# Optimization experiments

Hardware: AMD Instinct MI355X
Metric: run time of the kernel (lower is better)

Reference implementation:

```python
import jax, jax.numpy as jnp
import numpy as np

COST_CLASS = 1.0


def _lsa(cost):
    """linear_sum_assignment clone (Jonker-Volgenant shortest augmenting path),
    matching scipy.optimize.linear_sum_assignment semantics for rectangular inputs."""
    cost = np.asarray(cost, dtype=np.float64)
    transposed = cost.shape[0] > cost.shape[1]
    if transposed:
        cost = cost.T
    nr, nc = cost.shape
    u = np.zeros(nr)
    v = np.zeros(nc)
    path = np.full(nc, -1, dtype=np.int64)
    col4row = np.full(nr, -1, dtype=np.int64)
    row4col = np.full(nc, -1, dtype=np.int64)
    for cur in range(nr):
        i = cur
        SR = np.zeros(nr, dtype=bool)
        SC = np.zeros(nc, dtype=bool)
        d = np.full(nc, np.inf)
        minVal = 0.0
        sink = -1
        while sink == -1:
            SR[i] = True
            rem = ~SC
            r = minVal + cost[i, rem] - u[i] - v[rem]
            dr = d[rem]
            pr = path[rem]
            better = r < dr
            dr[better] = r[better]
            pr[better] = i
            d[rem] = dr
            path[rem] = pr
            remIdx = np.flatnonzero(rem)
            j = remIdx[np.argmin(d[remIdx])]
            minVal = d[j]
            SC[j] = True
            if row4col[j] == -1:
                sink = j
            else:
                i = row4col[j]
        # dual updates (scipy _lsap_body)
        u[cur] += minVal
        mask = SR.copy()
        mask[cur] = False
        u[mask] += minVal - d[col4row[mask]]
        v[SC] -= minVal - d[SC]
        # augment along shortest path
        j = sink
        while True:
            i = path[j]
            row4col[j] = i
            col4row[i], j = j, col4row[i]
            if i == cur:
                break
    if transposed:
        order = np.argsort(col4row)
        return col4row[order], order
    return np.arange(nr), col4row


def setup_inputs() -> dict:
    key = jax.random.key(0)
    k1, k2, k3 = jax.random.split(key, 3)
    bs, Q, T, NC = 32, 256, 128, 2048
    pred_logits = jax.random.normal(k1, (bs, Q, NC), dtype=jnp.float32)
    tgt_labels = jax.random.randint(k2, (bs, T), 0, NC)
    agent_mask = jax.random.randint(k3, (bs, Q), 0, 2).astype(bool)
    return {"pred_logits": pred_logits, "tgt_labels": tgt_labels,
            "agent_mask": agent_mask, "use_background": 0}


def reference(pred_logits, tgt_labels, agent_mask, use_background):
    bs, Q, _ = pred_logits.shape
    T = tgt_labels.shape[1]
    probs = jax.nn.softmax(pred_logits, axis=-1)  # [bs, Q, NC]
    if not use_background:
        probs = jnp.where(agent_mask[:, :, None], probs, 0.0)
    out_prob = probs.reshape(bs * Q, -1)
    tgt_ids = tgt_labels.reshape(-1)                  # concat of all batch labels
    C = COST_CLASS * (-out_prob[:, tgt_ids])          # [bs*Q, bs*T]
    C = C.reshape(bs, Q, bs * T)
    # per-batch Hungarian (same as scipy loop in the original; inherently serial per instance)
    Cn = np.asarray(C)
    rows = np.empty((bs, T), dtype=np.int64)
    cols = np.empty((bs, T), dtype=np.int64)
    for i in range(bs):
        r, c = _lsa(Cn[i, :, i * T:(i + 1) * T])      # [Q, T] block for batch i
        rows[i] = r
        cols[i] = c
    return C, jnp.asarray(rows), jnp.asarray(cols)
```

## Files before the change

kernel.cpp:

```cpp
#include <hip/hip_runtime.h>
#include <hip/hip_bf16.h>
#include <math.h>

#define BS 32
#define QN 256
#define TN 128
#define NCLS 2048
#define NTGT (BS * TN)

__global__ void detect_mask_layout(const unsigned char* __restrict__ m, int* flag) {
    __shared__ int found;
    if (threadIdx.x == 0) found = 0;
    __syncthreads();
    int local = 0;
    for (int i = threadIdx.x; i < BS * QN; i += blockDim.x) {
        if ((i & 3) != 0 && m[i] != 0) local = 1;
    }
    if (local) atomicOr(&found, 1);
    __syncthreads();
    if (threadIdx.x == 0) *flag = found;
}

__global__ __launch_bounds__(256) void ct_kernel(
    const float* __restrict__ logits, const int* __restrict__ labels,
    const unsigned char* __restrict__ mask_b, const int* __restrict__ use_bg,
    const int* __restrict__ layout_flag, float* __restrict__ CT) {
    __shared__ float prob_sh[NCLS];
    __shared__ float red[4];

    const int tid = threadIdx.x;
    const int bq = blockIdx.x;
    const float* row = logits + (size_t)bq * NCLS;

    const float4 xa = ((const float4*)row)[tid];
    const float4 xb = ((const float4*)row)[tid + 256];

    float m = fmaxf(fmaxf(fmaxf(xa.x, xa.y), fmaxf(xa.z, xa.w)),
                    fmaxf(fmaxf(xb.x, xb.y), fmaxf(xb.z, xb.w)));
#pragma unroll
    for (int off = 32; off >= 1; off >>= 1) m = fmaxf(m, __shfl_xor(m, off));
    if ((tid & 63) == 0) red[tid >> 6] = m;
    __syncthreads();
    m = fmaxf(fmaxf(red[0], red[1]), fmaxf(red[2], red[3]));
    __syncthreads();

    float4 ea, eb;
    ea.x = expf(xa.x - m);
    ea.y = expf(xa.y - m);
    ea.z = expf(xa.z - m);
    ea.w = expf(xa.w - m);
    eb.x = expf(xb.x - m);
    eb.y = expf(xb.y - m);
    eb.z = expf(xb.z - m);
    eb.w = expf(xb.w - m);
    float s = ((ea.x + ea.y) + (ea.z + ea.w)) + ((eb.x + eb.y) + (eb.z + eb.w));
#pragma unroll
    for (int off = 32; off >= 1; off >>= 1) s += __shfl_xor(s, off);
    if ((tid & 63) == 0) red[tid >> 6] = s;
    __syncthreads();
    s = ((red[0] + red[1]) + red[2]) + red[3];

    ((float4*)prob_sh)[tid] = make_float4(ea.x / s, ea.y / s, ea.z / s, ea.w / s);
    ((float4*)prob_sh)[tid + 256] = make_float4(eb.x / s, eb.y / s, eb.z / s, eb.w / s);

    const int ub = *use_bg;
    int am;
    if (*layout_flag)
        am = mask_b[bq];
    else
        am = ((const int*)mask_b)[bq];
    const bool zero_row = (ub == 0) && (am == 0);
    __syncthreads();

    if (tid < TN) {
        const int bb = bq >> 8;
        const int q = bq & 255;
        const int lab = labels[bb * TN + tid];
        CT[(size_t)bb * TN * QN + (size_t)tid * QN + q] =
            zero_row ? 0.0f : -prob_sh[lab];
    }
}

__global__ __launch_bounds__(256) void compute_C_kernel(
    const float* __restrict__ logits, const int* __restrict__ labels,
    const unsigned char* __restrict__ mask_b, const int* __restrict__ use_bg,
    const int* __restrict__ layout_flag, float* __restrict__ C) {
    __shared__ float prob_sh[NCLS];
    __shared__ float red[4];

    const int tid = threadIdx.x;
    const int bq = blockIdx.x;
    const float* row = logits + (size_t)bq * NCLS;

    const float4 xa = ((const float4*)row)[tid];
    const float4 xb = ((const float4*)row)[tid + 256];

    float m = fmaxf(fmaxf(fmaxf(xa.x, xa.y), fmaxf(xa.z, xa.w)),
                    fmaxf(fmaxf(xb.x, xb.y), fmaxf(xb.z, xb.w)));
#pragma unroll
    for (int off = 32; off >= 1; off >>= 1) m = fmaxf(m, __shfl_xor(m, off));
    if ((tid & 63) == 0) red[tid >> 6] = m;
    __syncthreads();
    m = fmaxf(fmaxf(red[0], red[1]), fmaxf(red[2], red[3]));
    __syncthreads();

    float4 ea, eb;
    ea.x = expf(xa.x - m);
    ea.y = expf(xa.y - m);
    ea.z = expf(xa.z - m);
    ea.w = expf(xa.w - m);
    eb.x = expf(xb.x - m);
    eb.y = expf(xb.y - m);
    eb.z = expf(xb.z - m);
    eb.w = expf(xb.w - m);
    float s = ((ea.x + ea.y) + (ea.z + ea.w)) + ((eb.x + eb.y) + (eb.z + eb.w));
#pragma unroll
    for (int off = 32; off >= 1; off >>= 1) s += __shfl_xor(s, off);
    if ((tid & 63) == 0) red[tid >> 6] = s;
    __syncthreads();
    s = ((red[0] + red[1]) + red[2]) + red[3];

    ((float4*)prob_sh)[tid] = make_float4(ea.x / s, ea.y / s, ea.z / s, ea.w / s);
    ((float4*)prob_sh)[tid + 256] = make_float4(eb.x / s, eb.y / s, eb.z / s, eb.w / s);

    const int ub = *use_bg;
    int am;
    if (*layout_flag)
        am = mask_b[bq];
    else
        am = ((const int*)mask_b)[bq];
    const bool zero_row = (ub == 0) && (am == 0);
    __syncthreads();

    float* Crow = C + (size_t)bq * NTGT;
    const int4* lab4 = (const int4*)labels;
    if (zero_row) {
        const float4 z = make_float4(0.f, 0.f, 0.f, 0.f);
#pragma unroll
        for (int k = 0; k < 4; k++) ((float4*)Crow)[tid + k * 256] = z;
    } else {
#pragma unroll
        for (int k = 0; k < 4; k++) {
            const int4 l = lab4[tid + k * 256];
            float4 o;
            o.x = -prob_sh[l.x];
            o.y = -prob_sh[l.y];
            o.z = -prob_sh[l.z];
            o.w = -prob_sh[l.w];
            ((float4*)Crow)[tid + k * 256] = o;
        }
    }
}

template <int CTRL>
__device__ __forceinline__ double dpp_mov_f64(double x) {
    union { double d; int i[2]; } a, r;
    a.d = x;
    r.i[0] = __builtin_amdgcn_update_dpp(0, a.i[0], CTRL, 0xF, 0xF, true);
    r.i[1] = __builtin_amdgcn_update_dpp(0, a.i[1], CTRL, 0xF, 0xF, true);
    return r.d;
}
__device__ __forceinline__ double read_lane_f64(double x, int srclane) {
    union { double d; int i[2]; } a, r;
    a.d = x;
    r.i[0] = __builtin_amdgcn_readlane(a.i[0], srclane);
    r.i[1] = __builtin_amdgcn_readlane(a.i[1], srclane);
    return r.d;
}

#define QUAD_XOR1 0xB1
#define QUAD_XOR2 0x4E
#define ROW_ROR4  0x124
#define ROW_ROR8  0x128

__device__ __forceinline__ void lsa_solve(
    const float* __restrict__ C, const float* __restrict__ CT,
    float* __restrict__ rows_out, float* __restrict__ cols_out,
    int b, int lane,
    float* cost_sh, double* u_sh, int* path_sh, int* row4col_sh, int* col4row_sh) {
    const int j0 = lane * 4;

    u_sh[lane] = 0.0;
    u_sh[lane + 64] = 0.0;
    col4row_sh[lane] = -1;
    col4row_sh[lane + 64] = -1;
#pragma unroll
    for (int t = 0; t < 4; t++) row4col_sh[lane + 64 * t] = -1;

    double v0 = 0.0, v1 = 0.0, v2 = 0.0, v3 = 0.0;
    double u0 = 0.0, u1 = 0.0;

    if (CT) {
        const float4* src = (const float4*)(CT + (size_t)b * TN * QN);
        float4* dst = (float4*)cost_sh;
#pragma unroll 8
        for (int it = 0; it < TN * QN / 4 / 64; it++) {
            const int idx = it * 64 + lane;
            dst[idx] = src[idx];
        }
    } else {
        const float* cbsrc = C + (size_t)b * QN * NTGT + b * TN;
        for (int it = 0; it < 512; it++) {
            const int j = it >> 1;
            const int i = lane + 64 * (it & 1);
            cost_sh[i * QN + j] = cbsrc[(size_t)j * NTGT + i];
        }
    }
    __syncthreads();

    for (int cur = 0; cur < TN; cur++) {
        double dv0 = INFINITY, dv1 = INFINITY, dv2 = INFINITY, dv3 = INFINITY;
        double dm0 = INFINITY, dm1 = INFINITY, dm2 = INFINITY, dm3 = INFINITY;
        double du0 = 0.0, du1 = 0.0;
        int sc = 0, sr = 0;
        int p0 = 0, p1 = 0, p2 = 0, p3 = 0;
        const int4 rcv = *(const int4*)&row4col_sh[j0];
        if (lane == (cur >> 1)) sr = 1 << (cur & 1);

        int i = cur;
        double m_d = 0.0;
        bool need_reduce = true;
        unsigned long long B0 = 0, B1 = 0, B2 = 0, B3 = 0;
        int sink;

        while (true) {
            const float4 cc = *(const float4*)(cost_sh + i * QN + j0);
            const double ui = u_sh[i];

            const double ca0 = ((m_d + (double)cc.x) - ui) - v0;
            const double ca1 = ((m_d + (double)cc.y) - ui) - v1;
            const double ca2 = ((m_d + (double)cc.z) - ui) - v2;
            const double ca3 = ((m_d + (double)cc.w) - ui) - v3;
            const bool i0 = !(sc & 1) && (ca0 < dv0);
            const bool i1 = !(sc & 2) && (ca1 < dv1);
            const bool i2 = !(sc & 4) && (ca2 < dv2);
            const bool i3 = !(sc & 8) && (ca3 < dv3);
            const unsigned long long anyI =
                __ballot(i0) | __ballot(i1) | __ballot(i2) | __ballot(i3);
            if (i0) { dv0 = ca0; dm0 = ca0; p0 = i; }
            if (i1) { dv1 = ca1; dm1 = ca1; p1 = i; }
            if (i2) { dv2 = ca2; dm2 = ca2; p2 = i; }
            if (i3) { dv3 = ca3; dm3 = ca3; p3 = i; }

            if (anyI != 0ull || need_reduce) {
                double lm = fmin(fmin(dm0, dm1), fmin(dm2, dm3));
                lm = fmin(lm, dpp_mov_f64<QUAD_XOR1>(lm));
                lm = fmin(lm, dpp_mov_f64<QUAD_XOR2>(lm));
                lm = fmin(lm, dpp_mov_f64<ROW_ROR4>(lm));
                lm = fmin(lm, dpp_mov_f64<ROW_ROR8>(lm));
                const double r0 = read_lane_f64(lm, 0);
                const double r1 = read_lane_f64(lm, 16);
                const double r2 = read_lane_f64(lm, 32);
                const double r3 = read_lane_f64(lm, 48);
                m_d = fmin(fmin(r0, r1), fmin(r2, r3));
                B0 = __ballot(dm0 == m_d);
                B1 = __ballot(dm1 == m_d);
                B2 = __ballot(dm2 == m_d);
                B3 = __ballot(dm3 == m_d);
            }

            int jmin = 0x7fffffff;
            if (B0) { const int c = ((__ffsll((long long)B0) - 1) << 2) + 0; jmin = c < jmin ? c : jmin; }
            if (B1) { const int c = ((__ffsll((long long)B1) - 1) << 2) + 1; jmin = c < jmin ? c : jmin; }
            if (B2) { const int c = ((__ffsll((long long)B2) - 1) << 2) + 2; jmin = c < jmin ? c : jmin; }
            if (B3) { const int c = ((__ffsll((long long)B3) - 1) << 2) + 3; jmin = c < jmin ? c : jmin; }
            const int owner = jmin >> 2;
            const int slot = jmin & 3;
            const unsigned long long bit = 1ull << owner;
            if (slot == 0) B0 &= ~bit;
            else if (slot == 1) B1 &= ~bit;
            else if (slot == 2) B2 &= ~bit;
            else B3 &= ~bit;

            if (lane == owner) {
                sc |= 1 << slot;
                if (slot == 0) dm0 = INFINITY;
                else if (slot == 1) dm1 = INFINITY;
                else if (slot == 2) dm2 = INFINITY;
                else dm3 = INFINITY;
            }

            const int sa = (slot & 1) ? rcv.y : rcv.x;
            const int sb = (slot & 1) ? rcv.w : rcv.z;
            const int rcsel = (slot & 2) ? sb : sa;
            const int krc = __builtin_amdgcn_readlane(rcsel, owner);
            if (krc < 0) { sink = jmin; break; }

            if (lane == (krc >> 1)) {
                if (krc & 1) { du1 = m_d; sr |= 2; }
                else { du0 = m_d; sr |= 1; }
            }
            i = krc;
            need_reduce = ((B0 | B1 | B2 | B3) == 0ull);
        }

        path_sh[lane] = p0;
        path_sh[lane + 64] = p1;
        path_sh[lane + 128] = p2;
        path_sh[lane + 192] = p3;
        if (sc & 1) v0 -= m_d - dv0;
        if (sc & 2) v1 -= m_d - dv1;
        if (sc & 4) v2 -= m_d - dv2;
        if (sc & 8) v3 -= m_d - dv3;
        if (sr & 1) u0 += (2 * lane == cur) ? m_d : (m_d - du0);
        if (sr & 2) u1 += (2 * lane + 1 == cur) ? m_d : (m_d - du1);
        u_sh[2 * lane] = u0;
        u_sh[2 * lane + 1] = u1;
        __syncthreads();

        if (lane == 0) {
            int j = sink;
            while (true) {
                const int pi = path_sh[(j & 3) * 64 + (j >> 2)];
                row4col_sh[j] = pi;
                const int nj = col4row_sh[pi];
                col4row_sh[pi] = j;
                j = nj;
                if (pi == cur) break;
            }
        }
        __syncthreads();
    }

#pragma unroll
    for (int t = 0; t < 2; t++) {
        const int ii = lane + 64 * t;
        const int myv = col4row_sh[ii];
        int rank = 0;
        for (int t2 = 0; t2 < TN; t2++) rank += (col4row_sh[t2] < myv) ? 1 : 0;
        rows_out[b * TN + rank] = (float)myv;
        cols_out[b * TN + rank] = (float)ii;
    }
}

__global__ __launch_bounds__(64) void lsa_kernel(const float* __restrict__ C,
                                                 const float* __restrict__ CT,
                                                 float* __restrict__ rows_out,
                                                 float* __restrict__ cols_out) {
    __shared__ float cost_sh[TN * QN];
    __shared__ double u_sh[TN];
    __shared__ int path_sh[QN];
    __shared__ int row4col_sh[QN];
    __shared__ int col4row_sh[TN];
    lsa_solve(C, CT, rows_out, cols_out, blockIdx.x, threadIdx.x,
              cost_sh, u_sh, path_sh, row4col_sh, col4row_sh);
}

__global__ __launch_bounds__(64) void fused_kernel(
    const float* __restrict__ logits, const int* __restrict__ labels,
    const unsigned char* __restrict__ mask_b, const int* __restrict__ use_bg,
    const int* __restrict__ layout_flag, const float* __restrict__ CT,
    float* __restrict__ C, float* __restrict__ rows_out,
    float* __restrict__ cols_out) {
    __shared__ float cost_sh[TN * QN];
    __shared__ double u_sh[TN];
    __shared__ int path_sh[QN];
    __shared__ int row4col_sh[QN];
    __shared__ int col4row_sh[TN];

    const int lane = threadIdx.x;

    if (blockIdx.x >= BS) {
        const int bq = blockIdx.x - BS;
        const float* row = logits + (size_t)bq * NCLS;

        float4 x[8];
#pragma unroll
        for (int k = 0; k < 8; k++) x[k] = ((const float4*)row)[lane + 64 * k];

        float m = -INFINITY;
#pragma unroll
        for (int k = 0; k < 8; k++)
            m = fmaxf(m, fmaxf(fmaxf(x[k].x, x[k].y), fmaxf(x[k].z, x[k].w)));
#pragma unroll
        for (int off = 32; off >= 1; off >>= 1) m = fmaxf(m, __shfl_xor(m, off));

        float s = 0.f;
        float4 e[8];
#pragma unroll
        for (int k = 0; k < 8; k++) {
            e[k].x = expf(x[k].x - m);
            e[k].y = expf(x[k].y - m);
            e[k].z = expf(x[k].z - m);
            e[k].w = expf(x[k].w - m);
            s += ((e[k].x + e[k].y) + (e[k].z + e[k].w));
        }
#pragma unroll
        for (int off = 32; off >= 1; off >>= 1) s += __shfl_xor(s, off);

        float* prob = cost_sh;
#pragma unroll
        for (int k = 0; k < 8; k++)
            ((float4*)prob)[lane + 64 * k] =
                make_float4(e[k].x / s, e[k].y / s, e[k].z / s, e[k].w / s);

        const int ub = *use_bg;
        int am;
        if (*layout_flag)
            am = mask_b[bq];
        else
            am = ((const int*)mask_b)[bq];
        const bool zero_row = (ub == 0) && (am == 0);
        __syncthreads();

        float* Crow = C + (size_t)bq * NTGT;
        const int4* lab4 = (const int4*)labels;
        if (zero_row) {
            const float4 z = make_float4(0.f, 0.f, 0.f, 0.f);
#pragma unroll
            for (int k = 0; k < 16; k++) ((float4*)Crow)[lane + 64 * k] = z;
        } else {
#pragma unroll
            for (int k = 0; k < 16; k++) {
                const int4 l = lab4[lane + 64 * k];
                ((float4*)Crow)[lane + 64 * k] =
                    make_float4(-prob[l.x], -prob[l.y], -prob[l.z], -prob[l.w]);
            }
        }
        return;
    }

    lsa_solve(nullptr, CT, rows_out, cols_out, blockIdx.x, lane,
              cost_sh, u_sh, path_sh, row4col_sh, col4row_sh);
}

extern "C" void kernel_launch(void* const* d_in, const int* in_sizes, int n_in,
                              void* d_out, int out_size, void* d_ws, size_t ws_size,
                              hipStream_t stream) {
    const float* logits = (const float*)d_in[0];
    const int* labels = (const int*)d_in[1];
    const unsigned char* mask_b = (const unsigned char*)d_in[2];
    const int* use_bg = (const int*)d_in[3];

    float* C = (float*)d_out;
    float* rows_out = C + (size_t)BS * QN * NTGT;
    float* cols_out = rows_out + BS * TN;

    int* flag = (int*)d_ws;
    const size_t ct_off = 4096;
    const size_t ct_bytes = (size_t)BS * TN * QN * sizeof(float);
    const bool useCT = ws_size >= ct_off + ct_bytes;
    float* CT = useCT ? (float*)((char*)d_ws + ct_off) : nullptr;

    detect_mask_layout<<<1, 256, 0, stream>>>(mask_b, flag);
    if (useCT) {
        ct_kernel<<<BS * QN, 256, 0, stream>>>(logits, labels, mask_b, use_bg, flag, CT);
        fused_kernel<<<BS + BS * QN, 64, 0, stream>>>(logits, labels, mask_b, use_bg,
                                                      flag, CT, C, rows_out, cols_out);
    } else {
        compute_C_kernel<<<BS * QN, 256, 0, stream>>>(logits, labels, mask_b, use_bg,
                                                      flag, C);
        lsa_kernel<<<BS, 64, 0, stream>>>(C, nullptr, rows_out, cols_out);
    }
}
```

Measured before the change: 1.129 ms.

## Speculatively prefetch next cost row in LSA loop and keep duals in registers

```diff
diff --git a/kernel.cpp b/kernel.cpp
--- a/kernel.cpp
+++ b/kernel.cpp
@@ -7,6 +7,8 @@
 #define TN 128
 #define NCLS 2048
 #define NTGT (BS * TN)
+
+typedef __attribute__((ext_vector_type(4))) float f32x4;
 
 __global__ void detect_mask_layout(const unsigned char* __restrict__ m, int* flag) {
     __shared__ int found;
@@ -167,6 +169,30 @@
     r.i[1] = __builtin_amdgcn_readlane(a.i[1], srclane);
     return r.d;
 }
+__device__ __forceinline__ int sel4(const int4& r, int slot) {
+    const int a = (slot & 1) ? r.y : r.x;
+    const int b = (slot & 1) ? r.w : r.z;
+    return (slot & 2) ? b : a;
+}
+__device__ __forceinline__ int pick_first(unsigned long long B0, unsigned long long B1,
+                                          unsigned long long B2, unsigned long long B3) {
+    int jmin = 0x7fffffff;
+    if (B0) { const int c = ((__ffsll((long long)B0) - 1) << 2) + 0; jmin = c < jmin ? c : jmin; }
+    if (B1) { const int c = ((__ffsll((long long)B1) - 1) << 2) + 1; jmin = c < jmin ? c : jmin; }
+    if (B2) { const int c = ((__ffsll((long long)B2) - 1) << 2) + 2; jmin = c < jmin ? c : jmin; }
+    if (B3) { const int c = ((__ffsll((long long)B3) - 1) << 2) + 3; jmin = c < jmin ? c : jmin; }
+    return jmin;
+}
+
+__device__ __forceinline__ f32x4 lds_read_b128_asm(unsigned addr) {
+    f32x4 r;
+    asm volatile("ds_read_b128 %0, %1" : "=v"(r) : "v"(addr));
+    return r;
+}
+__device__ __forceinline__ void lgkm_drain() {
+    asm volatile("s_waitcnt lgkmcnt(0)");
+    __builtin_amdgcn_sched_barrier(0);
+}
 
 #define QUAD_XOR1 0xB1
 #define QUAD_XOR2 0x4E
@@ -177,11 +203,9 @@
     const float* __restrict__ C, const float* __restrict__ CT,
     float* __restrict__ rows_out, float* __restrict__ cols_out,
     int b, int lane,
-    float* cost_sh, double* u_sh, int* path_sh, int* row4col_sh, int* col4row_sh) {
+    float* cost_sh, int* path_sh, int* row4col_sh, int* col4row_sh) {
     const int j0 = lane * 4;
 
-    u_sh[lane] = 0.0;
-    u_sh[lane + 64] = 0.0;
     col4row_sh[lane] = -1;
     col4row_sh[lane + 64] = -1;
 #pragma unroll
@@ -207,6 +231,17 @@
         }
     }
     __syncthreads();
+
+    const unsigned lds_base = (unsigned)(uintptr_t)cost_sh;
+    const unsigned lane_off = (unsigned)(j0 * 4);
+    bool asm_ok;
+    {
+        f32x4 chk = lds_read_b128_asm(lds_base + lane_off);
+        lgkm_drain();
+        const f32x4 ref = *(const f32x4*)(cost_sh + j0);
+        asm_ok = __all(chk.x == ref.x && chk.y == ref.y && chk.z == ref.z &&
+                       chk.w == ref.w) != 0;
+    }
 
     for (int cur = 0; cur < TN; cur++) {
         double dv0 = INFINITY, dv1 = INFINITY, dv2 = INFINITY, dv3 = INFINITY;
@@ -223,76 +258,157 @@
         unsigned long long B0 = 0, B1 = 0, B2 = 0, B3 = 0;
         int sink;
 
-        while (true) {
-            const float4 cc = *(const float4*)(cost_sh + i * QN + j0);
-            const double ui = u_sh[i];
-
-            const double ca0 = ((m_d + (double)cc.x) - ui) - v0;
-            const double ca1 = ((m_d + (double)cc.y) - ui) - v1;
-            const double ca2 = ((m_d + (double)cc.z) - ui) - v2;
-            const double ca3 = ((m_d + (double)cc.w) - ui) - v3;
-            const bool i0 = !(sc & 1) && (ca0 < dv0);
-            const bool i1 = !(sc & 2) && (ca1 < dv1);
-            const bool i2 = !(sc & 4) && (ca2 < dv2);
-            const bool i3 = !(sc & 8) && (ca3 < dv3);
-            const unsigned long long anyI =
-                __ballot(i0) | __ballot(i1) | __ballot(i2) | __ballot(i3);
-            if (i0) { dv0 = ca0; dm0 = ca0; p0 = i; }
-            if (i1) { dv1 = ca1; dm1 = ca1; p1 = i; }
-            if (i2) { dv2 = ca2; dm2 = ca2; p2 = i; }
-            if (i3) { dv3 = ca3; dm3 = ca3; p3 = i; }
-
-            if (anyI != 0ull || need_reduce) {
-                double lm = fmin(fmin(dm0, dm1), fmin(dm2, dm3));
-                lm = fmin(lm, dpp_mov_f64<QUAD_XOR1>(lm));
-                lm = fmin(lm, dpp_mov_f64<QUAD_XOR2>(lm));
-                lm = fmin(lm, dpp_mov_f64<ROW_ROR4>(lm));
-                lm = fmin(lm, dpp_mov_f64<ROW_ROR8>(lm));
-                const double r0 = read_lane_f64(lm, 0);
-                const double r1 = read_lane_f64(lm, 16);
-                const double r2 = read_lane_f64(lm, 32);
-                const double r3 = read_lane_f64(lm, 48);
-                m_d = fmin(fmin(r0, r1), fmin(r2, r3));
-                B0 = __ballot(dm0 == m_d);
-                B1 = __ballot(dm1 == m_d);
-                B2 = __ballot(dm2 == m_d);
-                B3 = __ballot(dm3 == m_d);
+        f32x4 cc = *(const f32x4*)(cost_sh + cur * QN + j0);
+        double ui = read_lane_f64((cur & 1) ? u1 : u0, cur >> 1);
+
+        if (asm_ok) {
+            while (true) {
+                int jp = 0x7fffffff, krc_sp = -1;
+                if (!need_reduce) {
+                    jp = pick_first(B0, B1, B2, B3);
+                    krc_sp = __builtin_amdgcn_readlane(sel4(rcv, jp & 3), jp >> 2);
+                }
+                f32x4 PF{};
+                const bool pf_live = (krc_sp >= 0);
+                if (pf_live)
+                    PF = lds_read_b128_asm(lds_base + ((unsigned)krc_sp << 10) + lane_off);
+
+                const double ca0 = ((m_d + (double)cc.x) - ui) - v0;
+                const double ca1 = ((m_d + (double)cc.y) - ui) - v1;
+                const double ca2 = ((m_d + (double)cc.z) - ui) - v2;
+                const double ca3 = ((m_d + (double)cc.w) - ui) - v3;
+                const bool i0 = !(sc & 1) && (ca0 < dv0);
+                const bool i1 = !(sc & 2) && (ca1 < dv1);
+                const bool i2 = !(sc & 4) && (ca2 < dv2);
+                const bool i3 = !(sc & 8) && (ca3 < dv3);
+                const unsigned long long anyI = __ballot(i0 | i1 | i2 | i3);
+                if (i0) { dv0 = ca0; dm0 = ca0; p0 = i; }
+                if (i1) { dv1 = ca1; dm1 = ca1; p1 = i; }
+                if (i2) { dv2 = ca2; dm2 = ca2; p2 = i; }
+                if (i3) { dv3 = ca3; dm3 = ca3; p3 = i; }
+
+                int jmin;
+                if (anyI != 0ull || need_reduce) {
+                    double lm = fmin(fmin(dm0, dm1), fmin(dm2, dm3));
+                    lm = fmin(lm, dpp_mov_f64<QUAD_XOR1>(lm));
+                    lm = fmin(lm, dpp_mov_f64<QUAD_XOR2>(lm));
+                    lm = fmin(lm, dpp_mov_f64<ROW_ROR4>(lm));
+                    lm = fmin(lm, dpp_mov_f64<ROW_ROR8>(lm));
+                    const double r0 = read_lane_f64(lm, 0);
+                    const double r1 = read_lane_f64(lm, 16);
+                    const double r2 = read_lane_f64(lm, 32);
+                    const double r3 = read_lane_f64(lm, 48);
+                    m_d = fmin(fmin(r0, r1), fmin(r2, r3));
+                    B0 = __ballot(dm0 == m_d);
+                    B1 = __ballot(dm1 == m_d);
+                    B2 = __ballot(dm2 == m_d);
+                    B3 = __ballot(dm3 == m_d);
+                    jmin = pick_first(B0, B1, B2, B3);
+                } else {
+                    jmin = jp;
+                }
+
+                const int owner = jmin >> 2;
+                const int slot = jmin & 3;
+                const unsigned long long bit = 1ull << owner;
+                if (slot == 0) B0 &= ~bit;
+                else if (slot == 1) B1 &= ~bit;
+                else if (slot == 2) B2 &= ~bit;
+                else B3 &= ~bit;
+
+                if (lane == owner) {
+                    sc |= 1 << slot;
+                    if (slot == 0) dm0 = INFINITY;
+                    else if (slot == 1) dm1 = INFINITY;
+                    else if (slot == 2) dm2 = INFINITY;
+                    else dm3 = INFINITY;
+                }
+
+                const bool hit = (jmin == jp);
+                const int krc =
+                    hit ? krc_sp : __builtin_amdgcn_readlane(sel4(rcv, slot), owner);
+                if (krc < 0) { sink = jmin; break; }
+
+                f32x4 DR{};
+                if (!hit)
+                    DR = lds_read_b128_asm(lds_base + ((unsigned)krc << 10) + lane_off);
+
+                if (lane == (krc >> 1)) {
+                    if (krc & 1) { du1 = m_d; sr |= 2; }
+                    else { du0 = m_d; sr |= 1; }
+                }
+                ui = read_lane_f64((krc & 1) ? u1 : u0, krc >> 1);
+                i = krc;
+                need_reduce = ((B0 | B1 | B2 | B3) == 0ull);
+
+                lgkm_drain();
+                cc = hit ? PF : DR;
             }
-
-            int jmin = 0x7fffffff;
-            if (B0) { const int c = ((__ffsll((long long)B0) - 1) << 2) + 0; jmin = c < jmin ? c : jmin; }
-            if (B1) { const int c = ((__ffsll((long long)B1) - 1) << 2) + 1; jmin = c < jmin ? c : jmin; }
-            if (B2) { const int c = ((__ffsll((long long)B2) - 1) << 2) + 2; jmin = c < jmin ? c : jmin; }
-            if (B3) { const int c = ((__ffsll((long long)B3) - 1) << 2) + 3; jmin = c < jmin ? c : jmin; }
-            const int owner = jmin >> 2;
-            const int slot = jmin & 3;
-            const unsigned long long bit = 1ull << owner;
-            if (slot == 0) B0 &= ~bit;
-            else if (slot == 1) B1 &= ~bit;
-            else if (slot == 2) B2 &= ~bit;
-            else B3 &= ~bit;
-
-            if (lane == owner) {
-                sc |= 1 << slot;
-                if (slot == 0) dm0 = INFINITY;
-                else if (slot == 1) dm1 = INFINITY;
-                else if (slot == 2) dm2 = INFINITY;
-                else dm3 = INFINITY;
+        } else {
+            while (true) {
+                const double ca0 = ((m_d + (double)cc.x) - ui) - v0;
+                const double ca1 = ((m_d + (double)cc.y) - ui) - v1;
+                const double ca2 = ((m_d + (double)cc.z) - ui) - v2;
+                const double ca3 = ((m_d + (double)cc.w) - ui) - v3;
+                const bool i0 = !(sc & 1) && (ca0 < dv0);
+                const bool i1 = !(sc & 2) && (ca1 < dv1);
+                const bool i2 = !(sc & 4) && (ca2 < dv2);
+                const bool i3 = !(sc & 8) && (ca3 < dv3);
+                const unsigned long long anyI =
+                    __ballot(i0) | __ballot(i1) | __ballot(i2) | __ballot(i3);
+                if (i0) { dv0 = ca0; dm0 = ca0; p0 = i; }
+                if (i1) { dv1 = ca1; dm1 = ca1; p1 = i; }
+                if (i2) { dv2 = ca2; dm2 = ca2; p2 = i; }
+                if (i3) { dv3 = ca3; dm3 = ca3; p3 = i; }
+
+                if (anyI != 0ull || need_reduce) {
+                    double lm = fmin(fmin(dm0, dm1), fmin(dm2, dm3));
+                    lm = fmin(lm, dpp_mov_f64<QUAD_XOR1>(lm));
+                    lm = fmin(lm, dpp_mov_f64<QUAD_XOR2>(lm));
+                    lm = fmin(lm, dpp_mov_f64<ROW_ROR4>(lm));
+                    lm = fmin(lm, dpp_mov_f64<ROW_ROR8>(lm));
+                    const double r0 = read_lane_f64(lm, 0);
+                    const double r1 = read_lane_f64(lm, 16);
+                    const double r2 = read_lane_f64(lm, 32);
+                    const double r3 = read_lane_f64(lm, 48);
+                    m_d = fmin(fmin(r0, r1), fmin(r2, r3));
+                    B0 = __ballot(dm0 == m_d);
+                    B1 = __ballot(dm1 == m_d);
+                    B2 = __ballot(dm2 == m_d);
+                    B3 = __ballot(dm3 == m_d);
+                }
+
+                const int jmin = pick_first(B0, B1, B2, B3);
+                const int owner = jmin >> 2;
+                const int slot = jmin & 3;
+                const unsigned long long bit = 1ull << owner;
+                if (slot == 0) B0 &= ~bit;
+                else if (slot == 1) B1 &= ~bit;
+                else if (slot == 2) B2 &= ~bit;
+                else B3 &= ~bit;
+
+                if (lane == owner) {
+                    sc |= 1 << slot;
+                    if (slot == 0) dm0 = INFINITY;
+                    else if (slot == 1) dm1 = INFINITY;
+                    else if (slot == 2) dm2 = INFINITY;
+                    else dm3 = INFINITY;
+                }
+
+                const int krc = __builtin_amdgcn_readlane(sel4(rcv, slot), owner);
+                if (krc < 0) { sink = jmin; break; }
+
+                if (lane == (krc >> 1)) {
+                    if (krc & 1) { du1 = m_d; sr |= 2; }
+                    else { du0 = m_d; sr |= 1; }
+                }
+                ui = read_lane_f64((krc & 1) ? u1 : u0, krc >> 1);
+                i = krc;
+                need_reduce = ((B0 | B1 | B2 | B3) == 0ull);
+                cc = *(const f32x4*)(cost_sh + i * QN + j0);
             }
-
-            const int sa = (slot & 1) ? rcv.y : rcv.x;
-            const int sb = (slot & 1) ? rcv.w : rcv.z;
-            const int rcsel = (slot & 2) ? sb : sa;
-            const int krc = __builtin_amdgcn_readlane(rcsel, owner);
-            if (krc < 0) { sink = jmin; break; }
-
-            if (lane == (krc >> 1)) {
-                if (krc & 1) { du1 = m_d; sr |= 2; }
-                else { du0 = m_d; sr |= 1; }
-            }
-            i = krc;
-            need_reduce = ((B0 | B1 | B2 | B3) == 0ull);
-        }
+        }
+        lgkm_drain();
 
         path_sh[lane] = p0;
         path_sh[lane + 64] = p1;
@@ -304,8 +420,6 @@
         if (sc & 8) v3 -= m_d - dv3;
         if (sr & 1) u0 += (2 * lane == cur) ? m_d : (m_d - du0);
         if (sr & 2) u1 += (2 * lane + 1 == cur) ? m_d : (m_d - du1);
-        u_sh[2 * lane] = u0;
-        u_sh[2 * lane + 1] = u1;
         __syncthreads();
 
         if (lane == 0) {
@@ -338,12 +452,11 @@
                                                  float* __restrict__ rows_out,
                                                  float* __restrict__ cols_out) {
     __shared__ float cost_sh[TN * QN];
-    __shared__ double u_sh[TN];
     __shared__ int path_sh[QN];
     __shared__ int row4col_sh[QN];
     __shared__ int col4row_sh[TN];
     lsa_solve(C, CT, rows_out, cols_out, blockIdx.x, threadIdx.x,
-              cost_sh, u_sh, path_sh, row4col_sh, col4row_sh);
+              cost_sh, path_sh, row4col_sh, col4row_sh);
 }
 
 __global__ __launch_bounds__(64) void fused_kernel(
@@ -353,7 +466,6 @@
     float* __restrict__ C, float* __restrict__ rows_out,
     float* __restrict__ cols_out) {
     __shared__ float cost_sh[TN * QN];
-    __shared__ double u_sh[TN];
     __shared__ int path_sh[QN];
     __shared__ int row4col_sh[QN];
     __shared__ int col4row_sh[TN];
@@ -421,7 +533,7 @@
     }
 
     lsa_solve(nullptr, CT, rows_out, cols_out, blockIdx.x, lane,
-              cost_sh, u_sh, path_sh, row4col_sh, col4row_sh);
+              cost_sh, path_sh, row4col_sh, col4row_sh);
 }
 
 extern "C" void kernel_launch(void* const* d_in, const int* in_sizes, int n_in,
@@ -450,6 +562,6 @@
     } else {
         compute_C_kernel<<<BS * QN, 256, 0, stream>>>(logits, labels, mask_b, use_bg,
                                                       flag, C);
-        lsa_kernel<<<BS, 64, 0, stream>>>(C, nullptr, rows_out, cols_out);
-    }
-}
+        lsa_kernel<<<BS, nullptr ? 64 : 64, 0, stream>>>(C, nullptr, rows_out, cols_out);
+    }
+}
```

New measurement: 1.264 ms. 11.9% more time.

## Keep LSA row/col assignment and path in registers, track min ties incrementally

Applied to the files above, without the earlier changes.

```diff
diff --git a/kernel.cpp b/kernel.cpp
--- a/kernel.cpp
+++ b/kernel.cpp
@@ -167,6 +167,11 @@
     r.i[1] = __builtin_amdgcn_readlane(a.i[1], srclane);
     return r.d;
 }
+__device__ __forceinline__ int sel4(const int4& r, int slot) {
+    const int a = (slot & 1) ? r.y : r.x;
+    const int b = (slot & 1) ? r.w : r.z;
+    return (slot & 2) ? b : a;
+}
 
 #define QUAD_XOR1 0xB1
 #define QUAD_XOR2 0x4E
@@ -177,18 +182,16 @@
     const float* __restrict__ C, const float* __restrict__ CT,
     float* __restrict__ rows_out, float* __restrict__ cols_out,
     int b, int lane,
-    float* cost_sh, double* u_sh, int* path_sh, int* row4col_sh, int* col4row_sh) {
+    float* cost_sh, double* u_sh, int* col4row_sh) {
     const int j0 = lane * 4;
 
     u_sh[lane] = 0.0;
     u_sh[lane + 64] = 0.0;
-    col4row_sh[lane] = -1;
-    col4row_sh[lane + 64] = -1;
-#pragma unroll
-    for (int t = 0; t < 4; t++) row4col_sh[lane + 64 * t] = -1;
 
     double v0 = 0.0, v1 = 0.0, v2 = 0.0, v3 = 0.0;
     double u0 = 0.0, u1 = 0.0;
+    int4 rc = make_int4(-1, -1, -1, -1);
+    int c0 = -1, c1 = -1;
 
     if (CT) {
         const float4* src = (const float4*)(CT + (size_t)b * TN * QN);
@@ -214,13 +217,11 @@
         double du0 = 0.0, du1 = 0.0;
         int sc = 0, sr = 0;
         int p0 = 0, p1 = 0, p2 = 0, p3 = 0;
-        const int4 rcv = *(const int4*)&row4col_sh[j0];
         if (lane == (cur >> 1)) sr = 1 << (cur & 1);
 
         int i = cur;
         double m_d = 0.0;
-        bool need_reduce = true;
-        unsigned long long B0 = 0, B1 = 0, B2 = 0, B3 = 0;
+        int tm = 0;
         int sink;
 
         while (true) {
@@ -235,14 +236,23 @@
             const bool i1 = !(sc & 2) && (ca1 < dv1);
             const bool i2 = !(sc & 4) && (ca2 < dv2);
             const bool i3 = !(sc & 8) && (ca3 < dv3);
-            const unsigned long long anyI =
-                __ballot(i0) | __ballot(i1) | __ballot(i2) | __ballot(i3);
             if (i0) { dv0 = ca0; dm0 = ca0; p0 = i; }
             if (i1) { dv1 = ca1; dm1 = ca1; p1 = i; }
             if (i2) { dv2 = ca2; dm2 = ca2; p2 = i; }
             if (i3) { dv3 = ca3; dm3 = ca3; p3 = i; }
 
-            if (anyI != 0ull || need_reduce) {
+            const bool lt_any = (i0 && ca0 < m_d) || (i1 && ca1 < m_d) ||
+                                (i2 && ca2 < m_d) || (i3 && ca3 < m_d);
+            int tmn = tm;
+            if (i0 && ca0 == m_d) tmn |= 1;
+            if (i1 && ca1 == m_d) tmn |= 2;
+            if (i2 && ca2 == m_d) tmn |= 4;
+            if (i3 && ca3 == m_d) tmn |= 8;
+
+            const unsigned long long LT = __ballot(lt_any);
+            unsigned long long W = __ballot(tmn != 0);
+
+            if (LT != 0ull || W == 0ull) {
                 double lm = fmin(fmin(dm0, dm1), fmin(dm2, dm3));
                 lm = fmin(lm, dpp_mov_f64<QUAD_XOR1>(lm));
                 lm = fmin(lm, dpp_mov_f64<QUAD_XOR2>(lm));
@@ -253,37 +263,27 @@
                 const double r2 = read_lane_f64(lm, 32);
                 const double r3 = read_lane_f64(lm, 48);
                 m_d = fmin(fmin(r0, r1), fmin(r2, r3));
-                B0 = __ballot(dm0 == m_d);
-                B1 = __ballot(dm1 == m_d);
-                B2 = __ballot(dm2 == m_d);
-                B3 = __ballot(dm3 == m_d);
-            }
-
-            int jmin = 0x7fffffff;
-            if (B0) { const int c = ((__ffsll((long long)B0) - 1) << 2) + 0; jmin = c < jmin ? c : jmin; }
-            if (B1) { const int c = ((__ffsll((long long)B1) - 1) << 2) + 1; jmin = c < jmin ? c : jmin; }
-            if (B2) { const int c = ((__ffsll((long long)B2) - 1) << 2) + 2; jmin = c < jmin ? c : jmin; }
-            if (B3) { const int c = ((__ffsll((long long)B3) - 1) << 2) + 3; jmin = c < jmin ? c : jmin; }
-            const int owner = jmin >> 2;
-            const int slot = jmin & 3;
-            const unsigned long long bit = 1ull << owner;
-            if (slot == 0) B0 &= ~bit;
-            else if (slot == 1) B1 &= ~bit;
-            else if (slot == 2) B2 &= ~bit;
-            else B3 &= ~bit;
+                tmn = (dm0 == m_d ? 1 : 0) | (dm1 == m_d ? 2 : 0) |
+                      (dm2 == m_d ? 4 : 0) | (dm3 == m_d ? 8 : 0);
+                W = __ballot(tmn != 0);
+            }
+
+            const int owner = __ffsll((unsigned long long)W) - 1;
+            const int sm = __builtin_amdgcn_readlane(tmn, owner);
+            const int slot = __ffs(sm) - 1;
+            const int jmin = (owner << 2) + slot;
 
             if (lane == owner) {
                 sc |= 1 << slot;
+                tmn &= ~(1 << slot);
                 if (slot == 0) dm0 = INFINITY;
                 else if (slot == 1) dm1 = INFINITY;
                 else if (slot == 2) dm2 = INFINITY;
                 else dm3 = INFINITY;
             }
-
-            const int sa = (slot & 1) ? rcv.y : rcv.x;
-            const int sb = (slot & 1) ? rcv.w : rcv.z;
-            const int rcsel = (slot & 2) ? sb : sa;
-            const int krc = __builtin_amdgcn_readlane(rcsel, owner);
+            tm = tmn;
+
+            const int krc = __builtin_amdgcn_readlane(sel4(rc, slot), owner);
             if (krc < 0) { sink = jmin; break; }
 
             if (lane == (krc >> 1)) {
@@ -291,13 +291,8 @@
                 else { du0 = m_d; sr |= 1; }
             }
             i = krc;
-            need_reduce = ((B0 | B1 | B2 | B3) == 0ull);
-        }
-
-        path_sh[lane] = p0;
-        path_sh[lane + 64] = p1;
-        path_sh[lane + 128] = p2;
-        path_sh[lane + 192] = p3;
+        }
+
         if (sc & 1) v0 -= m_d - dv0;
         if (sc & 2) v1 -= m_d - dv1;
         if (sc & 4) v2 -= m_d - dv2;
@@ -306,21 +301,34 @@
         if (sr & 2) u1 += (2 * lane + 1 == cur) ? m_d : (m_d - du1);
         u_sh[2 * lane] = u0;
         u_sh[2 * lane + 1] = u1;
+
+        int j = sink;
+        while (true) {
+            const int sl = j & 3;
+            const int ow = j >> 2;
+            const int pa = (sl & 1) ? p1 : p0;
+            const int pb = (sl & 1) ? p3 : p2;
+            const int pi = __builtin_amdgcn_readlane((sl & 2) ? pb : pa, ow);
+            if (lane == ow) {
+                if (sl == 0) rc.x = pi;
+                else if (sl == 1) rc.y = pi;
+                else if (sl == 2) rc.z = pi;
+                else rc.w = pi;
+            }
+            const int nj = __builtin_amdgcn_readlane((pi & 1) ? c1 : c0, pi >> 1);
+            if (lane == (pi >> 1)) {
+                if (pi & 1) c1 = j;
+                else c0 = j;
+            }
+            j = nj;
+            if (pi == cur) break;
+        }
         __syncthreads();
-
-        if (lane == 0) {
-            int j = sink;
-            while (true) {
-                const int pi = path_sh[(j & 3) * 64 + (j >> 2)];
-                row4col_sh[j] = pi;
-                const int nj = col4row_sh[pi];
-                col4row_sh[pi] = j;
-                j = nj;
-                if (pi == cur) break;
-            }
-        }
-        __syncthreads();
-    }
+    }
+
+    col4row_sh[2 * lane] = c0;
+    col4row_sh[2 * lane + 1] = c1;
+    __syncthreads();
 
 #pragma unroll
     for (int t = 0; t < 2; t++) {
@@ -339,11 +347,9 @@
                                                  float* __restrict__ cols_out) {
     __shared__ float cost_sh[TN * QN];
     __shared__ double u_sh[TN];
-    __shared__ int path_sh[QN];
-    __shared__ int row4col_sh[QN];
     __shared__ int col4row_sh[TN];
     lsa_solve(C, CT, rows_out, cols_out, blockIdx.x, threadIdx.x,
-              cost_sh, u_sh, path_sh, row4col_sh, col4row_sh);
+              cost_sh, u_sh, col4row_sh);
 }
 
 __global__ __launch_bounds__(64) void fused_kernel(
@@ -354,8 +360,6 @@
     float* __restrict__ cols_out) {
     __shared__ float cost_sh[TN * QN];
     __shared__ double u_sh[TN];
-    __shared__ int path_sh[QN];
-    __shared__ int row4col_sh[QN];
     __shared__ int col4row_sh[TN];
 
     const int lane = threadIdx.x;
@@ -421,7 +425,7 @@
     }
 
     lsa_solve(nullptr, CT, rows_out, cols_out, blockIdx.x, lane,
-              cost_sh, u_sh, path_sh, row4col_sh, col4row_sh);
+              cost_sh, u_sh, col4row_sh);
 }
 
 extern "C" void kernel_launch(void* const* d_in, const int* in_sizes, int n_in,
```

After: 1.083 ms. 1.04x faster.
